# Optimization experiments

Hardware: AMD Instinct MI355X
Metric: run time of the kernel (lower is better)

## Reference

```python
import jax, jax.numpy as jnp
import numpy as np

N = 50000
E = 800000
C_IN, C_HID, C_OUT = 128, 64, 1


def setup_inputs() -> dict:
    key = jax.random.key(0)
    ks = jax.random.split(key, 8)
    x = jax.random.normal(ks[0], (N, C_IN), dtype=jnp.float32)
    edge_index = jax.random.randint(ks[1], (2, E), 0, N, dtype=jnp.int64)
    # GCNConv linear params (glorot-ish scaling)
    W1 = jax.random.normal(ks[2], (C_IN, C_HID), dtype=jnp.float32) / np.sqrt(C_IN)
    b1 = jnp.zeros((C_HID,), dtype=jnp.float32)
    W2 = jax.random.normal(ks[3], (C_HID, C_HID), dtype=jnp.float32) / np.sqrt(C_HID)
    b2 = jnp.zeros((C_HID,), dtype=jnp.float32)
    W3 = jax.random.normal(ks[4], (C_HID, C_OUT), dtype=jnp.float32) / np.sqrt(C_HID)
    b3 = jnp.zeros((C_OUT,), dtype=jnp.float32)
    return {"x": x, "edge_index": edge_index, "W1": W1, "b1": b1,
            "W2": W2, "b2": b2, "W3": W3, "b3": b3}


def _gcn_norm(edge_index, num_nodes):
    # Add self-loops, compute symmetric normalization D^{-1/2} A D^{-1/2}
    loop = jnp.arange(num_nodes, dtype=edge_index.dtype)
    src = jnp.concatenate([edge_index[0], loop])  # message sources
    dst = jnp.concatenate([edge_index[1], loop])  # message targets
    ones = jnp.ones(src.shape[0], dtype=jnp.float32)
    deg = jax.ops.segment_sum(ones, dst, num_segments=num_nodes)
    dis = jnp.where(deg > 0, jax.lax.rsqrt(jnp.maximum(deg, 1.0)), 0.0)
    norm = dis[src] * dis[dst]  # [E+N]
    return src, dst, norm


def _gcn_conv(h, src, dst, norm, W, b, num_nodes):
    h = h @ W                                  # [N, C_out]
    msg = h[src] * norm[:, None]               # gather + scale, [E+N, C_out]
    out = jax.ops.segment_sum(msg, dst, num_segments=num_nodes)  # scatter-add
    return out + b


def reference(x, edge_index, W1, b1, W2, b2, W3, b3):
    num_nodes = x.shape[0]
    src, dst, norm = _gcn_norm(edge_index, num_nodes)
    leaky = lambda v: jnp.where(v >= 0, v, 0.01 * v)
    h = _gcn_conv(x, src, dst, norm, W1, b1, num_nodes)
    h = leaky(h)
    h = _gcn_conv(h, src, dst, norm, W2, b2, num_nodes)
    h = leaky(h)
    h = _gcn_conv(h, src, dst, norm, W3, b3, num_nodes)
    return h
```

## Files before the change

### kernel.cpp

```cpp
#include <hip/hip_runtime.h>

#define CIN 128
#define CHID 64
#define CSTRIDE 64

__device__ __forceinline__ float leaky(float v) { return v >= 0.f ? v : 0.01f * v; }
__device__ __forceinline__ float bcast(float v, int k) {
    return __int_as_float(__builtin_amdgcn_readlane(__float_as_int(v), k));
}
__device__ __forceinline__ void acc4(float4& a, const float4 v) {
    a.x += v.x; a.y += v.y; a.z += v.z; a.w += v.w;
}
__device__ __forceinline__ void xorred(float4& a) {
    a.x += __shfl_xor(a.x, 16, 64); a.y += __shfl_xor(a.y, 16, 64);
    a.z += __shfl_xor(a.z, 16, 64); a.w += __shfl_xor(a.w, 16, 64);
    a.x += __shfl_xor(a.x, 32, 64); a.y += __shfl_xor(a.y, 32, 64);
    a.z += __shfl_xor(a.z, 32, 64); a.w += __shfl_xor(a.w, 32, 64);
}

__global__ void k_deg(const int* __restrict__ dst, const int* __restrict__ src,
                      int* __restrict__ deg, unsigned short* __restrict__ csr, int E) {
    int e = blockIdx.x * 256 + threadIdx.x;
    if (e >= E) return;
    int d = dst[e];
    int slot = atomicAdd(&deg[d], 1);
    if (slot < CSTRIDE) csr[(d << 6) + slot] = (unsigned short)src[e];
}

__global__ __launch_bounds__(256) void k_gemm1(
    const float* __restrict__ x, const float* __restrict__ W,
    const int* __restrict__ deg, float* __restrict__ hp, int N) {
    const int wave = threadIdx.x >> 6, lane = threadIdx.x & 63;
    float w[CIN];
#pragma unroll
    for (int k = 0; k < CIN; ++k) w[k] = W[k * CHID + lane];
    const int stride = gridDim.x * 4;
    for (int n = blockIdx.x * 4 + wave; n < N; n += stride) {
        float x0 = x[(size_t)n * CIN + lane];
        float x1 = x[(size_t)n * CIN + 64 + lane];
        float acc0 = 0.f, acc1 = 0.f;
#pragma unroll
        for (int k = 0; k < 64; k += 2) {
            acc0 = fmaf(bcast(x0, k),     w[k],     acc0);
            acc1 = fmaf(bcast(x0, k + 1), w[k + 1], acc1);
        }
#pragma unroll
        for (int k = 0; k < 64; k += 2) {
            acc0 = fmaf(bcast(x1, k),     w[64 + k],     acc0);
            acc1 = fmaf(bcast(x1, k + 1), w[64 + k + 1], acc1);
        }
        float dn = rsqrtf((float)(deg[n] + 1));
        hp[(size_t)n * CHID + lane] = dn * (acc0 + acc1);
    }
}

__global__ __launch_bounds__(256) void kG1(
    const unsigned short* __restrict__ csr, const int* __restrict__ deg,
    const float* __restrict__ hp, const float* __restrict__ W2,
    const float* __restrict__ b1, float* __restrict__ hp2, int N) {
    const int wave = threadIdx.x >> 6, lane = threadIdx.x & 63;
    const int g = lane >> 4, sl = lane & 15;
    float w[CHID];
#pragma unroll
    for (int k = 0; k < CHID; ++k) w[k] = W2[k * CHID + lane];
    const float4 bb = ((const float4*)b1)[sl];
    const float4* __restrict__ hpq = (const float4*)hp;
    const int stride = gridDim.x * 4;
    const int n0 = blockIdx.x * 4 + wave;
    int d = 0, c0 = 0, c1 = 0, c2 = 0, c3 = 0;
    if (n0 < N) {
        d = deg[n0];
        int base = n0 << 6;
        c0 = csr[base + g];      c1 = csr[base + g + 4];
        c2 = csr[base + g + 8];  c3 = csr[base + g + 12];
    }
    for (int n = n0; n < N; n += stride) {
        const int n2 = n + stride;
        int dN = 0, e0 = 0, e1 = 0, e2 = 0, e3 = 0;
        if (n2 < N) {
            dN = deg[n2];
            int b2 = n2 << 6;
            e0 = csr[b2 + g];      e1 = csr[b2 + g + 4];
            e2 = csr[b2 + g + 8];  e3 = csr[b2 + g + 12];
        }
        const int dc = d, base = n << 6;
        float4 a0 = make_float4(0.f, 0.f, 0.f, 0.f), a1 = a0, a2 = a0, a3 = a0;
        if (g == 0) a0 = hpq[(size_t)n * 16 + sl];
        if (g < dc)      acc4(a0, hpq[(size_t)c0 * 16 + sl]);
        if (g + 4 < dc)  acc4(a1, hpq[(size_t)c1 * 16 + sl]);
        if (g + 8 < dc)  acc4(a2, hpq[(size_t)c2 * 16 + sl]);
        if (g + 12 < dc) acc4(a3, hpq[(size_t)c3 * 16 + sl]);
        for (int b = g + 16; b < dc; b += 16) {
            { int s = csr[base + b];      acc4(a0, hpq[(size_t)s * 16 + sl]); }
            if (b + 4 < dc)  { int s = csr[base + b + 4];  acc4(a1, hpq[(size_t)s * 16 + sl]); }
            if (b + 8 < dc)  { int s = csr[base + b + 8];  acc4(a2, hpq[(size_t)s * 16 + sl]); }
            if (b + 12 < dc) { int s = csr[base + b + 12]; acc4(a3, hpq[(size_t)s * 16 + sl]); }
        }
        acc4(a0, a1); acc4(a2, a3); acc4(a0, a2);
        xorred(a0);
        float dn = rsqrtf((float)(dc + 1));
        float4 gv;
        gv.x = leaky(dn * a0.x + bb.x);
        gv.y = leaky(dn * a0.y + bb.y);
        gv.z = leaky(dn * a0.z + bb.z);
        gv.w = leaky(dn * a0.w + bb.w);
        float acc0 = 0.f, acc1 = 0.f;
#pragma unroll
        for (int i = 0; i < 16; ++i) {
            acc0 = fmaf(bcast(gv.x, i), w[4 * i + 0], acc0);
            acc1 = fmaf(bcast(gv.y, i), w[4 * i + 1], acc1);
            acc0 = fmaf(bcast(gv.z, i), w[4 * i + 2], acc0);
            acc1 = fmaf(bcast(gv.w, i), w[4 * i + 3], acc1);
        }
        hp2[(size_t)n * CHID + lane] = dn * (acc0 + acc1);
        d = dN; c0 = e0; c1 = e1; c2 = e2; c3 = e3;
    }
}

__global__ __launch_bounds__(256) void kG2(
    const unsigned short* __restrict__ csr, const int* __restrict__ deg,
    const float* __restrict__ hp, const float* __restrict__ b2,
    const float* __restrict__ W3, float* __restrict__ hp3, int N) {
    const int wave = threadIdx.x >> 6, lane = threadIdx.x & 63;
    const int g = lane >> 4, sl = lane & 15;
    const float4 bb = ((const float4*)b2)[sl];
    const float4 w3 = ((const float4*)W3)[sl];
    const float4* __restrict__ hpq = (const float4*)hp;
    const int stride = gridDim.x * 4;
    const int n0 = blockIdx.x * 4 + wave;
    int d = 0, c0 = 0, c1 = 0, c2 = 0, c3 = 0;
    if (n0 < N) {
        d = deg[n0];
        int base = n0 << 6;
        c0 = csr[base + g];      c1 = csr[base + g + 4];
        c2 = csr[base + g + 8];  c3 = csr[base + g + 12];
    }
    for (int n = n0; n < N; n += stride) {
        const int n2 = n + stride;
        int dN = 0, e0 = 0, e1 = 0, e2 = 0, e3 = 0;
        if (n2 < N) {
            dN = deg[n2];
            int b2i = n2 << 6;
            e0 = csr[b2i + g];      e1 = csr[b2i + g + 4];
            e2 = csr[b2i + g + 8];  e3 = csr[b2i + g + 12];
        }
        const int dc = d, base = n << 6;
        float4 a0 = make_float4(0.f, 0.f, 0.f, 0.f), a1 = a0, a2 = a0, a3 = a0;
        if (g == 0) a0 = hpq[(size_t)n * 16 + sl];
        if (g < dc)      acc4(a0, hpq[(size_t)c0 * 16 + sl]);
        if (g + 4 < dc)  acc4(a1, hpq[(size_t)c1 * 16 + sl]);
        if (g + 8 < dc)  acc4(a2, hpq[(size_t)c2 * 16 + sl]);
        if (g + 12 < dc) acc4(a3, hpq[(size_t)c3 * 16 + sl]);
        for (int b = g + 16; b < dc; b += 16) {
            { int s = csr[base + b];      acc4(a0, hpq[(size_t)s * 16 + sl]); }
            if (b + 4 < dc)  { int s = csr[base + b + 4];  acc4(a1, hpq[(size_t)s * 16 + sl]); }
            if (b + 8 < dc)  { int s = csr[base + b + 8];  acc4(a2, hpq[(size_t)s * 16 + sl]); }
            if (b + 12 < dc) { int s = csr[base + b + 12]; acc4(a3, hpq[(size_t)s * 16 + sl]); }
        }
        acc4(a0, a1); acc4(a2, a3); acc4(a0, a2);
        xorred(a0);
        float dn = rsqrtf((float)(dc + 1));
        float t = leaky(dn * a0.x + bb.x) * w3.x
                + leaky(dn * a0.y + bb.y) * w3.y
                + leaky(dn * a0.z + bb.z) * w3.z
                + leaky(dn * a0.w + bb.w) * w3.w;
        t += __shfl_xor(t, 1, 64); t += __shfl_xor(t, 2, 64);
        t += __shfl_xor(t, 4, 64); t += __shfl_xor(t, 8, 64);
        if (lane == 0) hp3[n] = dn * t;
        d = dN; c0 = e0; c1 = e1; c2 = e2; c3 = e3;
    }
}

__global__ void kG3(const unsigned short* __restrict__ csr, const int* __restrict__ deg,
                    const float* __restrict__ hp3, const float* __restrict__ b3,
                    float* __restrict__ out, int N) {
    int t = blockIdx.x * 256 + threadIdx.x;
    int node = t >> 4, sl = t & 15;
    if (node >= N) return;
    int d = deg[node], base = node << 6;
    float acc = (sl == 0) ? hp3[node] : 0.f;
    for (int i = sl; i < d; i += 16) acc += hp3[(int)csr[base + i]];
#pragma unroll
    for (int off = 8; off > 0; off >>= 1) acc += __shfl_down(acc, off, 16);
    if (sl == 0) out[node] = rsqrtf((float)(d + 1)) * acc + b3[0];
}

extern "C" void kernel_launch(void* const* d_in, const int* in_sizes, int n_in,
                              void* d_out, int out_size, void* d_ws, size_t ws_size,
                              hipStream_t stream) {
    const float* x  = (const float*)d_in[0];
    const int*   ei = (const int*)d_in[1];
    const float* W1 = (const float*)d_in[2];
    const float* b1 = (const float*)d_in[3];
    const float* W2 = (const float*)d_in[4];
    const float* b2 = (const float*)d_in[5];
    const float* W3 = (const float*)d_in[6];
    const float* b3 = (const float*)d_in[7];

    const int N = in_sizes[0] / CIN;
    const int E = in_sizes[1] / 2;
    const int* src = ei;
    const int* dst = ei + E;

    char* w = (char*)d_ws;
    auto take = [&](size_t bytes) { char* p = w; w += (bytes + 255) & ~(size_t)255; return p; };
    int*            deg = (int*)take((size_t)N * 4);
    unsigned short* csr = (unsigned short*)take((size_t)N * CSTRIDE * 2);
    float*          A   = (float*)take((size_t)N * CHID * 4);
    float*          B   = (float*)take((size_t)N * CHID * 4);
    float*          hp3 = (float*)take((size_t)N * 4);

    hipMemsetAsync(deg, 0, (size_t)N * 4, stream);

    k_deg  <<<(E + 255) / 256, 256, 0, stream>>>(dst, src, deg, csr, E);
    k_gemm1<<<1024, 256, 0, stream>>>(x, W1, deg, A, N);
    kG1    <<<2048, 256, 0, stream>>>(csr, deg, A, W2, b1, B, N);
    kG2    <<<2048, 256, 0, stream>>>(csr, deg, B, b2, W3, hp3, N);
    kG3    <<<(N * 16 + 255) / 256, 256, 0, stream>>>(csr, deg, hp3, b3, (float*)d_out, N);
}
```

Measured before the change: 233.5 us.

## Shard degree/CSR build by destination range and prefetch packed 32-bit neighbor pairs

The degree/CSR build kernel becomes a grid-stride loop in which blocks are split into 8 shards by destination node range. Each shard scans all edges but only does atomics for destinations in its range, which aims to keep atomic and CSR write traffic local to fewer cache slices or XCDs. This costs 8x reads of the dst array. The gather kernels now prefetch the first 32 neighbor indices as packed 32-bit pairs into 8 accumulators, which cuts the number of per-edge csr loads for typical degrees (~16) at the cost of more registers.

```diff
diff --git a/kernel.cpp b/kernel.cpp
--- a/kernel.cpp
+++ b/kernel.cpp
@@ -19,12 +19,21 @@
 }
 
 __global__ void k_deg(const int* __restrict__ dst, const int* __restrict__ src,
-                      int* __restrict__ deg, unsigned short* __restrict__ csr, int E) {
-    int e = blockIdx.x * 256 + threadIdx.x;
-    if (e >= E) return;
-    int d = dst[e];
-    int slot = atomicAdd(&deg[d], 1);
-    if (slot < CSTRIDE) csr[(d << 6) + slot] = (unsigned short)src[e];
+                      int* __restrict__ deg, unsigned short* __restrict__ csr,
+                      int E, int nps, int N) {
+    const int shard = blockIdx.x & 7;
+    const int chunk = blockIdx.x >> 3;
+    const int nchunks = gridDim.x >> 3;
+    const int lo = shard * nps;
+    const int hi = min(lo + nps, N);
+    const int estride = nchunks * 256;
+    for (int e = chunk * 256 + threadIdx.x; e < E; e += estride) {
+        int d = dst[e];
+        if (d >= lo && d < hi) {
+            int slot = atomicAdd(&deg[d], 1);
+            if (slot < CSTRIDE) csr[(d << 6) + slot] = (unsigned short)src[e];
+        }
+    }
 }
 
 __global__ __launch_bounds__(256) void k_gemm1(
@@ -53,6 +62,31 @@
         hp[(size_t)n * CHID + lane] = dn * (acc0 + acc1);
     }
 }
+
+#define GATHER_BODY(dc, base, nrow)                                              \
+    float4 A0 = make_float4(0.f,0.f,0.f,0.f), A1=A0,A2=A0,A3=A0,A4=A0,A5=A0,A6=A0,A7=A0; \
+    if (g == 0) A0 = hpq[(size_t)(nrow) * 16 + sl];                              \
+    { int s0 = c0 & 0xffff, s1 = c0 >> 16;                                       \
+      if (2*g     < dc) acc4(A0, hpq[(size_t)s0 * 16 + sl]);                     \
+      if (2*g + 1 < dc) acc4(A1, hpq[(size_t)s1 * 16 + sl]); }                   \
+    { int s0 = c1 & 0xffff, s1 = c1 >> 16;                                       \
+      if (2*g + 8 < dc) acc4(A2, hpq[(size_t)s0 * 16 + sl]);                     \
+      if (2*g + 9 < dc) acc4(A3, hpq[(size_t)s1 * 16 + sl]); }                   \
+    { int s0 = c2 & 0xffff, s1 = c2 >> 16;                                       \
+      if (2*g + 16 < dc) acc4(A4, hpq[(size_t)s0 * 16 + sl]);                    \
+      if (2*g + 17 < dc) acc4(A5, hpq[(size_t)s1 * 16 + sl]); }                  \
+    { int s0 = c3 & 0xffff, s1 = c3 >> 16;                                       \
+      if (2*g + 24 < dc) acc4(A6, hpq[(size_t)s0 * 16 + sl]);                    \
+      if (2*g + 25 < dc) acc4(A7, hpq[(size_t)s1 * 16 + sl]); }                  \
+    for (int b = 32 + g; b < dc; b += 16) {                                      \
+        { int s = csr[(base) + b];      acc4(A0, hpq[(size_t)s * 16 + sl]); }    \
+        if (b + 4 < dc)  { int s = csr[(base) + b + 4];  acc4(A1, hpq[(size_t)s * 16 + sl]); } \
+        if (b + 8 < dc)  { int s = csr[(base) + b + 8];  acc4(A2, hpq[(size_t)s * 16 + sl]); } \
+        if (b + 12 < dc) { int s = csr[(base) + b + 12]; acc4(A3, hpq[(size_t)s * 16 + sl]); } \
+    }                                                                            \
+    acc4(A0, A1); acc4(A2, A3); acc4(A4, A5); acc4(A6, A7);                      \
+    acc4(A0, A2); acc4(A4, A6); acc4(A0, A4);                                    \
+    xorred(A0);
 
 __global__ __launch_bounds__(256) void kG1(
     const unsigned short* __restrict__ csr, const int* __restrict__ deg,
@@ -65,45 +99,33 @@
     for (int k = 0; k < CHID; ++k) w[k] = W2[k * CHID + lane];
     const float4 bb = ((const float4*)b1)[sl];
     const float4* __restrict__ hpq = (const float4*)hp;
+    const unsigned int* __restrict__ csr32 = (const unsigned int*)csr;
     const int stride = gridDim.x * 4;
     const int n0 = blockIdx.x * 4 + wave;
-    int d = 0, c0 = 0, c1 = 0, c2 = 0, c3 = 0;
+    int d = 0; unsigned int c0 = 0, c1 = 0, c2 = 0, c3 = 0;
     if (n0 < N) {
         d = deg[n0];
-        int base = n0 << 6;
-        c0 = csr[base + g];      c1 = csr[base + g + 4];
-        c2 = csr[base + g + 8];  c3 = csr[base + g + 12];
+        int b32 = n0 << 5;
+        c0 = csr32[b32 + g];      c1 = csr32[b32 + g + 4];
+        c2 = csr32[b32 + g + 8];  c3 = csr32[b32 + g + 12];
     }
     for (int n = n0; n < N; n += stride) {
         const int n2 = n + stride;
-        int dN = 0, e0 = 0, e1 = 0, e2 = 0, e3 = 0;
+        int dN = 0; unsigned int e0 = 0, e1 = 0, e2 = 0, e3 = 0;
         if (n2 < N) {
             dN = deg[n2];
-            int b2 = n2 << 6;
-            e0 = csr[b2 + g];      e1 = csr[b2 + g + 4];
-            e2 = csr[b2 + g + 8];  e3 = csr[b2 + g + 12];
+            int b32 = n2 << 5;
+            e0 = csr32[b32 + g];      e1 = csr32[b32 + g + 4];
+            e2 = csr32[b32 + g + 8];  e3 = csr32[b32 + g + 12];
         }
         const int dc = d, base = n << 6;
-        float4 a0 = make_float4(0.f, 0.f, 0.f, 0.f), a1 = a0, a2 = a0, a3 = a0;
-        if (g == 0) a0 = hpq[(size_t)n * 16 + sl];
-        if (g < dc)      acc4(a0, hpq[(size_t)c0 * 16 + sl]);
-        if (g + 4 < dc)  acc4(a1, hpq[(size_t)c1 * 16 + sl]);
-        if (g + 8 < dc)  acc4(a2, hpq[(size_t)c2 * 16 + sl]);
-        if (g + 12 < dc) acc4(a3, hpq[(size_t)c3 * 16 + sl]);
-        for (int b = g + 16; b < dc; b += 16) {
-            { int s = csr[base + b];      acc4(a0, hpq[(size_t)s * 16 + sl]); }
-            if (b + 4 < dc)  { int s = csr[base + b + 4];  acc4(a1, hpq[(size_t)s * 16 + sl]); }
-            if (b + 8 < dc)  { int s = csr[base + b + 8];  acc4(a2, hpq[(size_t)s * 16 + sl]); }
-            if (b + 12 < dc) { int s = csr[base + b + 12]; acc4(a3, hpq[(size_t)s * 16 + sl]); }
-        }
-        acc4(a0, a1); acc4(a2, a3); acc4(a0, a2);
-        xorred(a0);
+        GATHER_BODY(dc, base, n)
         float dn = rsqrtf((float)(dc + 1));
         float4 gv;
-        gv.x = leaky(dn * a0.x + bb.x);
-        gv.y = leaky(dn * a0.y + bb.y);
-        gv.z = leaky(dn * a0.z + bb.z);
-        gv.w = leaky(dn * a0.w + bb.w);
+        gv.x = leaky(dn * A0.x + bb.x);
+        gv.y = leaky(dn * A0.y + bb.y);
+        gv.z = leaky(dn * A0.z + bb.z);
+        gv.w = leaky(dn * A0.w + bb.w);
         float acc0 = 0.f, acc1 = 0.f;
 #pragma unroll
         for (int i = 0; i < 16; ++i) {
@@ -126,49 +148,39 @@
     const float4 bb = ((const float4*)b2)[sl];
     const float4 w3 = ((const float4*)W3)[sl];
     const float4* __restrict__ hpq = (const float4*)hp;
+    const unsigned short* __restrict__ csrl = csr;
+    const unsigned int* __restrict__ csr32 = (const unsigned int*)csr;
     const int stride = gridDim.x * 4;
     const int n0 = blockIdx.x * 4 + wave;
-    int d = 0, c0 = 0, c1 = 0, c2 = 0, c3 = 0;
+    int d = 0; unsigned int c0 = 0, c1 = 0, c2 = 0, c3 = 0;
     if (n0 < N) {
         d = deg[n0];
-        int base = n0 << 6;
-        c0 = csr[base + g];      c1 = csr[base + g + 4];
-        c2 = csr[base + g + 8];  c3 = csr[base + g + 12];
+        int b32 = n0 << 5;
+        c0 = csr32[b32 + g];      c1 = csr32[b32 + g + 4];
+        c2 = csr32[b32 + g + 8];  c3 = csr32[b32 + g + 12];
     }
     for (int n = n0; n < N; n += stride) {
         const int n2 = n + stride;
-        int dN = 0, e0 = 0, e1 = 0, e2 = 0, e3 = 0;
+        int dN = 0; unsigned int e0 = 0, e1 = 0, e2 = 0, e3 = 0;
         if (n2 < N) {
             dN = deg[n2];
-            int b2i = n2 << 6;
-            e0 = csr[b2i + g];      e1 = csr[b2i + g + 4];
-            e2 = csr[b2i + g + 8];  e3 = csr[b2i + g + 12];
+            int b32 = n2 << 5;
+            e0 = csr32[b32 + g];      e1 = csr32[b32 + g + 4];
+            e2 = csr32[b32 + g + 8];  e3 = csr32[b32 + g + 12];
         }
         const int dc = d, base = n << 6;
-        float4 a0 = make_float4(0.f, 0.f, 0.f, 0.f), a1 = a0, a2 = a0, a3 = a0;
-        if (g == 0) a0 = hpq[(size_t)n * 16 + sl];
-        if (g < dc)      acc4(a0, hpq[(size_t)c0 * 16 + sl]);
-        if (g + 4 < dc)  acc4(a1, hpq[(size_t)c1 * 16 + sl]);
-        if (g + 8 < dc)  acc4(a2, hpq[(size_t)c2 * 16 + sl]);
-        if (g + 12 < dc) acc4(a3, hpq[(size_t)c3 * 16 + sl]);
-        for (int b = g + 16; b < dc; b += 16) {
-            { int s = csr[base + b];      acc4(a0, hpq[(size_t)s * 16 + sl]); }
-            if (b + 4 < dc)  { int s = csr[base + b + 4];  acc4(a1, hpq[(size_t)s * 16 + sl]); }
-            if (b + 8 < dc)  { int s = csr[base + b + 8];  acc4(a2, hpq[(size_t)s * 16 + sl]); }
-            if (b + 12 < dc) { int s = csr[base + b + 12]; acc4(a3, hpq[(size_t)s * 16 + sl]); }
-        }
-        acc4(a0, a1); acc4(a2, a3); acc4(a0, a2);
-        xorred(a0);
+        GATHER_BODY(dc, base, n)
         float dn = rsqrtf((float)(dc + 1));
-        float t = leaky(dn * a0.x + bb.x) * w3.x
-                + leaky(dn * a0.y + bb.y) * w3.y
-                + leaky(dn * a0.z + bb.z) * w3.z
-                + leaky(dn * a0.w + bb.w) * w3.w;
+        float t = leaky(dn * A0.x + bb.x) * w3.x
+                + leaky(dn * A0.y + bb.y) * w3.y
+                + leaky(dn * A0.z + bb.z) * w3.z
+                + leaky(dn * A0.w + bb.w) * w3.w;
         t += __shfl_xor(t, 1, 64); t += __shfl_xor(t, 2, 64);
         t += __shfl_xor(t, 4, 64); t += __shfl_xor(t, 8, 64);
         if (lane == 0) hp3[n] = dn * t;
         d = dN; c0 = e0; c1 = e1; c2 = e2; c3 = e3;
     }
+    (void)csrl;
 }
 
 __global__ void kG3(const unsigned short* __restrict__ csr, const int* __restrict__ deg,
@@ -201,6 +213,7 @@
     const int E = in_sizes[1] / 2;
     const int* src = ei;
     const int* dst = ei + E;
+    const int nps = (N + 7) / 8;
 
     char* w = (char*)d_ws;
     auto take = [&](size_t bytes) { char* p = w; w += (bytes + 255) & ~(size_t)255; return p; };
@@ -212,7 +225,7 @@
 
     hipMemsetAsync(deg, 0, (size_t)N * 4, stream);
 
-    k_deg  <<<(E + 255) / 256, 256, 0, stream>>>(dst, src, deg, csr, E);
+    k_deg  <<<2048, 256, 0, stream>>>(dst, src, deg, csr, E, nps, N);
     k_gemm1<<<1024, 256, 0, stream>>>(x, W1, deg, A, N);
     kG1    <<<2048, 256, 0, stream>>>(csr, deg, A, W2, b1, B, N);
     kG2    <<<2048, 256, 0, stream>>>(csr, deg, B, b2, W3, hp3, N);
```

After: 242.8 us. 4.0% more time.
